# Kernel tuning notes

Measured on AMD Instinct MI355X. Metric: run time of the kernel, lower is better.

Reference implementation:

```python
import jax, jax.numpy as jnp
import numpy as np

V, N, K, D = 100000, 20000, 32, 128
NEG = -1e9  # masked logit value


def setup_inputs() -> dict:
    key = jax.random.key(0)
    ks = jax.random.split(key, 8)
    return {
        "nodes": jax.random.randint(ks[0], (N,), 0, V),
        "neigh_idx": jax.random.randint(ks[1], (N, K), 0, V),
        "degrees": jax.random.randint(ks[2], (N,), 0, K + 1),
        "u2e": jax.random.normal(ks[3], (V, D), dtype=jnp.float32),
        "W1": jax.random.normal(ks[4], (2 * D, D), dtype=jnp.float32) * 0.05,
        "b1": jnp.zeros((D,), jnp.float32),
        "W2": jax.random.normal(ks[5], (D, D), dtype=jnp.float32) * 0.05,
        "b2": jnp.zeros((D,), jnp.float32),
        "W3": jax.random.normal(ks[6], (D, 1), dtype=jnp.float32) * 0.05,
        "b3": jnp.zeros((1,), jnp.float32),
    }


def reference(nodes, neigh_idx, degrees, u2e, W1, b1, W2, b2, W3, b3):
    self_feats = u2e[nodes]                      # [N, D]
    e_u = u2e[neigh_idx]                         # [N, K, D] ragged gather (padded)
    # Attention MLP: cat(neighbor, self) -> relu -> relu -> scalar logit
    x = jnp.concatenate([e_u, jnp.broadcast_to(self_feats[:, None, :], (e_u.shape[0], K, D))], axis=-1)  # [N, K, 2D]
    h = jax.nn.relu(x @ W1 + b1)                 # [N, K, D]
    h = jax.nn.relu(h @ W2 + b2)                 # [N, K, D]
    logits = (h @ W3 + b3)[..., 0]               # [N, K]
    mask = jnp.arange(K)[None, :] < degrees[:, None]
    att = jax.nn.softmax(jnp.where(mask, logits, NEG), axis=-1)  # softmax over neighbors
    agg = jnp.einsum("nk,nkd->nd", att, e_u)     # attention-weighted neighbor sum
    out = jnp.where(degrees[:, None] > 0, (agg + self_feats) * 0.5, self_feats)
    return out
```

## Files before the change

### kernel.cpp

```cpp
#include <hip/hip_runtime.h>
#include <hip/hip_bf16.h>

#define KK 32
#define DD 128
#define NEGV (-1e9f)
#define SE 136
#define PREP_BLKS 2048

typedef __attribute__((ext_vector_type(8))) short bf16x8;
typedef __attribute__((ext_vector_type(4))) float f32x4;

__device__ __forceinline__ unsigned short f2bf(float f) {
    union { float f; unsigned u; } v; v.f = f;
    unsigned r = v.u + 0x7fffu + ((v.u >> 16) & 1u);
    return (unsigned short)(r >> 16);
}
__device__ __forceinline__ float bf2f(unsigned short h) {
    union { unsigned u; float f; } v; v.u = ((unsigned)h) << 16;
    return v.f;
}
__device__ __forceinline__ unsigned pk2(float x, float y) {
    union { __hip_bfloat162 h; unsigned u; } c;
    c.h = __float22bfloat162_rn(float2{x, y});
    return c.u;
}

__global__ __launch_bounds__(256) void prep_kernel(
    const float* __restrict__ u2e, const float* __restrict__ W1, const float* __restrict__ W2,
    unsigned short* __restrict__ u2e_bf, unsigned short* __restrict__ W1t,
    unsigned short* __restrict__ W2t, const int u2e_blocks, const long Vd)
{
    const int b = blockIdx.x;
    if (b < u2e_blocks) {
        const long stride = (long)u2e_blocks * 256 * 8;
        for (long i = ((long)b * 256 + threadIdx.x) * 8; i < Vd; i += stride) {
            const float4 v0 = *(const float4*)(u2e + i);
            const float4 v1 = *(const float4*)(u2e + i + 4);
            uint4 p;
            p.x = pk2(v0.x, v0.y); p.y = pk2(v0.z, v0.w);
            p.z = pk2(v1.x, v1.y); p.w = pk2(v1.z, v1.w);
            *(uint4*)(u2e_bf + i) = p;
        }
    } else {
        const int id = (b - u2e_blocks) * 256 + threadIdx.x;
        if (id < 256 * 128) {
            const int n = id >> 8, k = id & 255;
            W1t[id] = f2bf(W1[k * DD + n]);
        } else {
            const int j = id - 256 * 128;
            const int n = j >> 7, k = j & 127;
            W2t[j] = f2bf(W2[k * DD + n]);
        }
    }
}

template<bool BF>
__global__ __launch_bounds__(256, 2) void ppagg_mfma(
    const int* __restrict__ nodes, const int* __restrict__ neigh,
    const int* __restrict__ degrees, const float* __restrict__ u2e,
    const unsigned short* __restrict__ u2e_bf,
    const unsigned short* __restrict__ W1t, const unsigned short* __restrict__ W2t,
    const float* __restrict__ b1, const float* __restrict__ b2,
    const float* __restrict__ W3, const float* __restrict__ b3,
    float* __restrict__ out, const int Nn)
{
    __shared__ __align__(16) unsigned short s_A[128 * SE];
    __shared__ __align__(16) unsigned short s_B[128 * SE];
    __shared__ __align__(16) unsigned short s_x8[8 * DD];
    __shared__ __align__(16) float s_selfc[8 * 128];
    __shared__ __align__(16) float s_b2w3[256];
    __shared__ float s_part[4][128];
    __shared__ float s_att[128];

    const int tid  = threadIdx.x;
    const int w    = tid >> 6;
    const int lane = tid & 63;
    const int ln   = lane & 15;
    const int q    = lane >> 4;

    const int nb = blockIdx.x * 8;
    const int r  = tid & 127;
    const int h  = tid >> 7;

    int idxA, idxB, vA, vB;
    {
        int ng0 = nb + (r >> 5);       if (ng0 >= Nn) ng0 = Nn - 1;
        int ng1 = nb + 4 + (r >> 5);   if (ng1 >= Nn) ng1 = Nn - 1;
        idxA = neigh[ng0 * KK + (r & 31)];
        idxB = neigh[ng1 * KK + (r & 31)];
        vA = (r & 31) < degrees[ng0];
        vB = (r & 31) < degrees[ng1];
    }

    auto stage = [&](unsigned short* buf, int idx, int v) {
        unsigned short* dst = buf + r * SE + h * 64;
        if (BF && v) {
            const uint4* src = (const uint4*)(u2e_bf + (long)idx * DD + h * 64);
            #pragma unroll
            for (int c = 0; c < 8; ++c) *(uint4*)(dst + c * 8) = src[c];
        } else if (!BF && v) {
            const float4* src = (const float4*)(u2e + (long)idx * DD + h * 64);
            #pragma unroll
            for (int c8 = 0; c8 < 8; ++c8) {
                const float4 v0 = src[c8 * 2];
                const float4 v1 = src[c8 * 2 + 1];
                uint4 p;
                p.x = pk2(v0.x, v0.y); p.y = pk2(v0.z, v0.w);
                p.z = pk2(v1.x, v1.y); p.w = pk2(v1.z, v1.w);
                *(uint4*)(dst + c8 * 8) = p;
            }
        } else {
            const uint4 z = {0u, 0u, 0u, 0u};
            #pragma unroll
            for (int c = 0; c < 8; ++c) *(uint4*)(dst + c * 8) = z;
        }
    };

    stage(s_A, idxA, vA);

    {
        int gn = nb + (tid >> 5); if (gn >= Nn) gn = Nn - 1;
        const int g = tid >> 5, p = tid & 31;
        const float4 v = *(const float4*)(u2e + (long)nodes[gn] * DD + p * 4);
        *(unsigned*)(s_x8 + g * DD + p * 4)     = pk2(v.x, v.y);
        *(unsigned*)(s_x8 + g * DD + p * 4 + 2) = pk2(v.z, v.w);
        s_b2w3[tid] = (tid < 128) ? b2[tid] : W3[tid - 128];
    }

    float2 self0, self1;
    {
        int n0 = nb + w;       if (n0 >= Nn) n0 = Nn - 1;
        int n1 = nb + 4 + w;   if (n1 >= Nn) n1 = Nn - 1;
        self0 = *(const float2*)(u2e + (long)nodes[n0] * DD + lane * 2);
        self1 = *(const float2*)(u2e + (long)nodes[n1] * DD + lane * 2);
    }

    bf16x8 b1f[4][2], b2f[4][2];
    float b1c[2];
    const int c0 = w * 32 + ln;
    const int c1 = c0 + 16;
    #pragma unroll
    for (int kk = 0; kk < 4; ++kk) {
        b1f[kk][0] = *(const bf16x8*)(W1t + c0 * 256 + kk * 32 + q * 8);
        b1f[kk][1] = *(const bf16x8*)(W1t + c1 * 256 + kk * 32 + q * 8);
        b2f[kk][0] = *(const bf16x8*)(W2t + c0 * 128 + kk * 32 + q * 8);
        b2f[kk][1] = *(const bf16x8*)(W2t + c1 * 128 + kk * 32 + q * 8);
    }
    b1c[0] = b1[c0]; b1c[1] = b1[c1];
    const float b3v = b3[0];

    __syncthreads();

    {
        f32x4 a0 = (f32x4){0.f,0.f,0.f,0.f}, a1 = (f32x4){0.f,0.f,0.f,0.f};
        #pragma unroll
        for (int kk = 0; kk < 4; ++kk) {
            const bf16x8 av = *(const bf16x8*)(s_x8 + (ln & 7) * DD + kk * 32 + q * 8);
            const bf16x8 w0 = *(const bf16x8*)(W1t + c0 * 256 + 128 + kk * 32 + q * 8);
            const bf16x8 w1 = *(const bf16x8*)(W1t + c1 * 256 + 128 + kk * 32 + q * 8);
            a0 = __builtin_amdgcn_mfma_f32_16x16x32_bf16(av, w0, a0, 0, 0, 0);
            a1 = __builtin_amdgcn_mfma_f32_16x16x32_bf16(av, w1, a1, 0, 0, 0);
        }
        if (q < 2) {
            #pragma unroll
            for (int rr = 0; rr < 4; ++rr) {
                s_selfc[(q * 4 + rr) * 128 + c0] = a0[rr] + b1c[0];
                s_selfc[(q * 4 + rr) * 128 + c1] = a1[rr] + b1c[1];
            }
        }
    }
    __syncthreads();

    #pragma unroll
    for (int it = 0; it < 2; ++it) {
        unsigned short* E = it ? s_B : s_A;
        unsigned short* H = it ? s_A : s_B;
        const int gbase = nb + it * 4;
        const float2 selfv = it ? self1 : self0;

        if (it == 1) __syncthreads();

        f32x4 acc[8][2];
        #pragma unroll
        for (int mt = 0; mt < 8; ++mt) {
            acc[mt][0] = (f32x4){0.f, 0.f, 0.f, 0.f};
            acc[mt][1] = (f32x4){0.f, 0.f, 0.f, 0.f};
        }
        #pragma unroll
        for (int kk = 0; kk < 4; ++kk) {
            bf16x8 a[8];
            #pragma unroll
            for (int mt = 0; mt < 8; ++mt)
                a[mt] = *(const bf16x8*)(E + (mt * 16 + ln) * SE + kk * 32 + q * 8);
            #pragma unroll
            for (int mt = 0; mt < 8; ++mt) {
                acc[mt][0] = __builtin_amdgcn_mfma_f32_16x16x32_bf16(b1f[kk][0], a[mt], acc[mt][0], 0, 0, 0);
                acc[mt][1] = __builtin_amdgcn_mfma_f32_16x16x32_bf16(b1f[kk][1], a[mt], acc[mt][1], 0, 0, 0);
            }
        }
        #pragma unroll
        for (int mt = 0; mt < 8; ++mt) {
            const int node = it * 4 + (mt >> 1);
            #pragma unroll
            for (int nt = 0; nt < 2; ++nt) {
                const int nb4 = w * 32 + nt * 16 + q * 4;
                const f32x4 sc = *(const f32x4*)(s_selfc + node * 128 + nb4);
                uint2 pw;
                pw.x = pk2(fmaxf(acc[mt][nt][0] + sc[0], 0.f),
                           fmaxf(acc[mt][nt][1] + sc[1], 0.f));
                pw.y = pk2(fmaxf(acc[mt][nt][2] + sc[2], 0.f),
                           fmaxf(acc[mt][nt][3] + sc[3], 0.f));
                *(uint2*)(H + (mt * 16 + ln) * SE + nb4) = pw;
            }
        }
        __syncthreads();

        f32x4 acc2[8][2];
        #pragma unroll
        for (int mt = 0; mt < 8; ++mt) {
            acc2[mt][0] = (f32x4){0.f, 0.f, 0.f, 0.f};
            acc2[mt][1] = (f32x4){0.f, 0.f, 0.f, 0.f};
        }
        #pragma unroll
        for (int kk = 0; kk < 4; ++kk) {
            bf16x8 a[8];
            #pragma unroll
            for (int mt = 0; mt < 8; ++mt)
                a[mt] = *(const bf16x8*)(H + (mt * 16 + ln) * SE + kk * 32 + q * 8);
            #pragma unroll
            for (int mt = 0; mt < 8; ++mt) {
                acc2[mt][0] = __builtin_amdgcn_mfma_f32_16x16x32_bf16(b2f[kk][0], a[mt], acc2[mt][0], 0, 0, 0);
                acc2[mt][1] = __builtin_amdgcn_mfma_f32_16x16x32_bf16(b2f[kk][1], a[mt], acc2[mt][1], 0, 0, 0);
            }
        }
        {
            const f32x4 b2v0 = *(const f32x4*)(s_b2w3 + w * 32 + q * 4);
            const f32x4 b2v1 = *(const f32x4*)(s_b2w3 + w * 32 + 16 + q * 4);
            const f32x4 w3v0 = *(const f32x4*)(s_b2w3 + 128 + w * 32 + q * 4);
            const f32x4 w3v1 = *(const f32x4*)(s_b2w3 + 128 + w * 32 + 16 + q * 4);
            #pragma unroll
            for (int mt = 0; mt < 8; ++mt) {
                float pl = 0.f;
                #pragma unroll
                for (int rr = 0; rr < 4; ++rr) {
                    pl = fmaf(fmaxf(acc2[mt][0][rr] + b2v0[rr], 0.f), w3v0[rr], pl);
                    pl = fmaf(fmaxf(acc2[mt][1][rr] + b2v1[rr], 0.f), w3v1[rr], pl);
                }
                pl += __shfl_xor(pl, 16);
                pl += __shfl_xor(pl, 32);
                if (lane < 16) s_part[w][mt * 16 + ln] = pl;
            }
        }
        __syncthreads();

        if (it == 0) stage(s_B, idxB, vB);

        if (tid < 128) {
            const int row = tid;
            const float logit = s_part[0][row] + s_part[1][row] + s_part[2][row] + s_part[3][row] + b3v;
            int ng = gbase + (row >> 5);
            if (ng >= Nn) ng = Nn - 1;
            const int deg = degrees[ng];
            const float ml = ((row & 31) < deg) ? logit : NEGV;
            float mx = ml;
            #pragma unroll
            for (int off = 16; off > 0; off >>= 1) mx = fmaxf(mx, __shfl_xor(mx, off));
            const float e = __expf(ml - mx);
            float ssum = e;
            #pragma unroll
            for (int off = 16; off > 0; off >>= 1) ssum += __shfl_xor(ssum, off);
            s_att[row] = e / ssum;
        }
        __syncthreads();

        {
            const int ng = gbase + w;
            const int degw = (ng < Nn) ? degrees[ng] : 0;
            float ax = 0.f, ay = 0.f;
            for (int k = 0; k < degw; ++k) {
                const float a = s_att[w * KK + k];
                const unsigned pe = *(const unsigned*)(E + (w * KK + k) * SE + lane * 2);
                ax = fmaf(a, bf2f((unsigned short)(pe & 0xffffu)), ax);
                ay = fmaf(a, bf2f((unsigned short)(pe >> 16)), ay);
            }
            if (ng < Nn) {
                float2 o;
                o.x = (degw > 0) ? 0.5f * (ax + selfv.x) : selfv.x;
                o.y = (degw > 0) ? 0.5f * (ay + selfv.y) : selfv.y;
                *(float2*)(out + (long)ng * DD + lane * 2) = o;
            }
        }
    }
}

extern "C" void kernel_launch(void* const* d_in, const int* in_sizes, int n_in,
                              void* d_out, int out_size, void* d_ws, size_t ws_size,
                              hipStream_t stream) {
    const int*   nodes   = (const int*)d_in[0];
    const int*   neigh   = (const int*)d_in[1];
    const int*   degrees = (const int*)d_in[2];
    const float* u2e     = (const float*)d_in[3];
    const float* W1      = (const float*)d_in[4];
    const float* b1      = (const float*)d_in[5];
    const float* W2      = (const float*)d_in[6];
    const float* b2      = (const float*)d_in[7];
    const float* W3      = (const float*)d_in[8];
    const float* b3      = (const float*)d_in[9];
    float* out = (float*)d_out;

    const int  Nn = in_sizes[0];
    const long Vd = (long)in_sizes[3];

    unsigned short* W1t = (unsigned short*)d_ws;
    unsigned short* W2t = W1t + 256 * 128;
    unsigned short* u2e_bf = W2t + 128 * 128;

    const size_t need_bf = (size_t)(256 * 128 + 128 * 128) * 2 + (size_t)Vd * 2;
    const bool use_bf = (ws_size >= need_bf) && (Vd % 8 == 0);
    const int u2e_blocks = use_bf ? PREP_BLKS : 0;

    prep_kernel<<<u2e_blocks + 192, 256, 0, stream>>>(u2e, W1, W2, u2e_bf, W1t, W2t,
                                                      u2e_blocks, Vd);

    const int grid = (Nn + 7) / 8;
    if (use_bf)
        ppagg_mfma<true><<<grid, 256, 0, stream>>>(nodes, neigh, degrees, u2e, u2e_bf,
                                                   W1t, W2t, b1, b2, W3, b3, out, Nn);
    else
        ppagg_mfma<false><<<grid, 256, 0, stream>>>(nodes, neigh, degrees, u2e, nullptr,
                                                    W1t, W2t, b1, b2, W3, b3, out, Nn);
}
```

Baseline: 204.2 us.

## Process sixteen nodes per block with ping-pong staged neighbor tiles

Each block now handles 16 nodes in four iterations instead of 8 in two. The A/B LDS buffers alternate, and the next neighbor tile is staged while the current one is consumed. Self features and self-GEMM results are refilled mid-loop. This spreads the per-block cost of loading W1/W2 register fragments and setup over twice as many nodes, but halves the grid and may worsen tail balance across CUs.

```diff
diff --git a/kernel.cpp b/kernel.cpp
--- a/kernel.cpp
+++ b/kernel.cpp
@@ -78,19 +78,9 @@
     const int ln   = lane & 15;
     const int q    = lane >> 4;
 
-    const int nb = blockIdx.x * 8;
+    const int nb = blockIdx.x * 16;
     const int r  = tid & 127;
     const int h  = tid >> 7;
-
-    int idxA, idxB, vA, vB;
-    {
-        int ng0 = nb + (r >> 5);       if (ng0 >= Nn) ng0 = Nn - 1;
-        int ng1 = nb + 4 + (r >> 5);   if (ng1 >= Nn) ng1 = Nn - 1;
-        idxA = neigh[ng0 * KK + (r & 31)];
-        idxB = neigh[ng1 * KK + (r & 31)];
-        vA = (r & 31) < degrees[ng0];
-        vB = (r & 31) < degrees[ng1];
-    }
 
     auto stage = [&](unsigned short* buf, int idx, int v) {
         unsigned short* dst = buf + r * SE + h * 64;
@@ -115,25 +105,25 @@
             for (int c = 0; c < 8; ++c) *(uint4*)(dst + c * 8) = z;
         }
     };
-
-    stage(s_A, idxA, vA);
-
-    {
-        int gn = nb + (tid >> 5); if (gn >= Nn) gn = Nn - 1;
+    auto load_idx = [&](int t, int& oi, int& ov) {
+        int ng = nb + t * 4 + (r >> 5); if (ng >= Nn) ng = Nn - 1;
+        oi = neigh[ng * KK + (r & 31)];
+        ov = (r & 31) < degrees[ng];
+    };
+    auto fill_x8 = [&](int off) {
+        int gn = nb + off + (tid >> 5); if (gn >= Nn) gn = Nn - 1;
         const int g = tid >> 5, p = tid & 31;
         const float4 v = *(const float4*)(u2e + (long)nodes[gn] * DD + p * 4);
         *(unsigned*)(s_x8 + g * DD + p * 4)     = pk2(v.x, v.y);
         *(unsigned*)(s_x8 + g * DD + p * 4 + 2) = pk2(v.z, v.w);
-        s_b2w3[tid] = (tid < 128) ? b2[tid] : W3[tid - 128];
-    }
-
-    float2 self0, self1;
-    {
-        int n0 = nb + w;       if (n0 >= Nn) n0 = Nn - 1;
-        int n1 = nb + 4 + w;   if (n1 >= Nn) n1 = Nn - 1;
-        self0 = *(const float2*)(u2e + (long)nodes[n0] * DD + lane * 2);
-        self1 = *(const float2*)(u2e + (long)nodes[n1] * DD + lane * 2);
-    }
+    };
+
+    int idx0, v0;
+    load_idx(0, idx0, v0);
+    stage(s_A, idx0, v0);
+
+    fill_x8(0);
+    if (tid < 256) s_b2w3[tid] = (tid < 128) ? b2[tid] : W3[tid - 128];
 
     bf16x8 b1f[4][2], b2f[4][2];
     float b1c[2];
@@ -149,9 +139,7 @@
     b1c[0] = b1[c0]; b1c[1] = b1[c1];
     const float b3v = b3[0];
 
-    __syncthreads();
-
-    {
+    auto self_gemm = [&]() {
         f32x4 a0 = (f32x4){0.f,0.f,0.f,0.f}, a1 = (f32x4){0.f,0.f,0.f,0.f};
         #pragma unroll
         for (int kk = 0; kk < 4; ++kk) {
@@ -168,17 +156,27 @@
                 s_selfc[(q * 4 + rr) * 128 + c1] = a1[rr] + b1c[1];
             }
         }
-    }
+    };
+
     __syncthreads();
+    self_gemm();
+    __syncthreads();
 
     #pragma unroll
-    for (int it = 0; it < 2; ++it) {
-        unsigned short* E = it ? s_B : s_A;
-        unsigned short* H = it ? s_A : s_B;
+    for (int it = 0; it < 4; ++it) {
+        unsigned short* E = (it & 1) ? s_B : s_A;
+        unsigned short* H = (it & 1) ? s_A : s_B;
         const int gbase = nb + it * 4;
-        const float2 selfv = it ? self1 : self0;
-
-        if (it == 1) __syncthreads();
+
+        if (it > 0) __syncthreads();
+
+        int nIdx = 0, nV = 0;
+        if (it < 3) load_idx(it + 1, nIdx, nV);
+        float2 selfv;
+        {
+            int ng = gbase + w; if (ng >= Nn) ng = Nn - 1;
+            selfv = *(const float2*)(u2e + (long)nodes[ng] * DD + lane * 2);
+        }
 
         f32x4 acc[8][2];
         #pragma unroll
@@ -200,11 +198,11 @@
         }
         #pragma unroll
         for (int mt = 0; mt < 8; ++mt) {
-            const int node = it * 4 + (mt >> 1);
+            const int slot = (it & 1) * 4 + (mt >> 1);
             #pragma unroll
             for (int nt = 0; nt < 2; ++nt) {
                 const int nb4 = w * 32 + nt * 16 + q * 4;
-                const f32x4 sc = *(const f32x4*)(s_selfc + node * 128 + nb4);
+                const f32x4 sc = *(const f32x4*)(s_selfc + slot * 128 + nb4);
                 uint2 pw;
                 pw.x = pk2(fmaxf(acc[mt][nt][0] + sc[0], 0.f),
                            fmaxf(acc[mt][nt][1] + sc[1], 0.f));
@@ -253,7 +251,9 @@
         }
         __syncthreads();
 
-        if (it == 0) stage(s_B, idxB, vB);
+        if (it < 3) stage(H, nIdx, nV);
+        if (it == 0) fill_x8(8);
+        if (it == 1) self_gemm();
 
         if (tid < 128) {
             const int row = tid;
@@ -322,7 +322,7 @@
     prep_kernel<<<u2e_blocks + 192, 256, 0, stream>>>(u2e, W1, W2, u2e_bf, W1t, W2t,
                                                       u2e_blocks, Vd);
 
-    const int grid = (Nn + 7) / 8;
+    const int grid = (Nn + 15) / 16;
     if (use_bf)
         ppagg_mfma<true><<<grid, 256, 0, stream>>>(nodes, neigh, degrees, u2e, u2e_bf,
                                                    W1t, W2t, b1, b2, W3, b3, out, Nn);
```

Result: no change. 206.0 us (+0.9%).
